# Kernel tuning notes

Hardware: AMD Instinct MI355X
Metric: run time of the kernel (lower is better)

The kernel has to match this reference:

```python
import jax, jax.numpy as jnp
import numpy as np

UNITS = 128
Q_DIM = 256
V_DIM = 256
BATCH = 128
SEQ = 4096


def setup_inputs() -> dict:
    key = jax.random.key(0)
    ks = jax.random.split(key, 8)
    query = jax.random.normal(ks[0], (BATCH, Q_DIM), dtype=jnp.float32)
    values = jax.random.normal(ks[1], (BATCH, SEQ, V_DIM), dtype=jnp.float32)
    # Dense params (glorot-ish scale)
    W1 = jax.random.normal(ks[2], (Q_DIM, UNITS), dtype=jnp.float32) * (1.0 / np.sqrt(Q_DIM))
    b1 = jnp.zeros((UNITS,), dtype=jnp.float32)
    W2 = jax.random.normal(ks[3], (V_DIM, UNITS), dtype=jnp.float32) * (1.0 / np.sqrt(V_DIM))
    b2 = jnp.zeros((UNITS,), dtype=jnp.float32)
    Wv = jax.random.normal(ks[4], (UNITS, 1), dtype=jnp.float32) * (1.0 / np.sqrt(UNITS))
    bv = jnp.zeros((1,), dtype=jnp.float32)
    return {"query": query, "values": values, "W1": W1, "b1": b1,
            "W2": W2, "b2": b2, "Wv": Wv, "bv": bv}


def reference(query, values, W1, b1, W2, b2, Wv, bv):
    # q_proj: [B, 1, U]; v_proj: [B, S, U]
    q_proj = (query @ W1 + b1)[:, None, :]
    v_proj = jnp.einsum('bsd,du->bsu', values, W2) + b2
    # score: [B, S, 1]
    score = jnp.tanh(q_proj + v_proj) @ Wv + bv
    attention_weights = jax.nn.softmax(score, axis=1)  # softmax over seq_len
    context = jnp.sum(attention_weights * values, axis=1)  # [B, V_DIM]
    return (context, attention_weights)
```

## Files before the change

kernel.cpp:

```cpp
#include <hip/hip_runtime.h>

#define B_ 128
#define S_ 4096
#define D_ 256
#define U_ 128
#define SC_ 128
#define CH_ 32

typedef _Float16 half8 __attribute__((ext_vector_type(8)));
typedef _Float16 half4_t __attribute__((ext_vector_type(4)));
typedef float f32x4 __attribute__((ext_vector_type(4)));


__global__ void qp_kernel(const float* __restrict__ query,
                          const float* __restrict__ W1,
                          const float* __restrict__ b1,
                          const float* __restrict__ b2,
                          float* __restrict__ qp) {
  const int idx = blockIdx.x * 256 + threadIdx.x;
  const int b = idx >> 7;
  const int u = idx & 127;
  float acc = b1[u] + b2[u];
  const float* q = query + b * D_;
  #pragma unroll 8
  for (int d = 0; d < D_; ++d) acc += q[d] * W1[d * U_ + u];
  qp[idx] = acc;
}

__global__ void w2t_kernel(const float* __restrict__ W2,
                           _Float16* __restrict__ w2t) {
  const int idx = blockIdx.x * 256 + threadIdx.x;
  const int u = idx >> 8;
  const int d = idx & 255;
  w2t[idx] = (_Float16)W2[d * U_ + u];
}


__global__ __launch_bounds__(256, 1)
void main_kernel(const float* __restrict__ values,
                 const float* __restrict__ qp,
                 const _Float16* __restrict__ w2t,
                 const float* __restrict__ Wv,
                 const float* __restrict__ bv,
                 float* __restrict__ scores,
                 float* __restrict__ part) {
  __shared__ _Float16 Alds[SC_][264];
  __shared__ _Float16 Blds[U_][264];
  __shared__ float sb[2][SC_];
  __shared__ float score_sh[SC_];
  __shared__ float p_sh[SC_];
  __shared__ float qp_sh[U_];
  __shared__ float wv_sh[U_];
  __shared__ float ctxpart[8][D_];
  __shared__ float red[4];

  const int t = threadIdx.x;
  const int bid = blockIdx.x;
  const int b = bid >> 5;
  const int s0 = (bid & 31) * SC_;

  const f32x4* __restrict__ vsrc =
      (const f32x4*)(values + ((size_t)b * S_ + s0) * D_);
  #pragma unroll 8
  for (int i = 0; i < 32; ++i) {
    const int idx = t + i * 256;
    const int row = idx >> 6;
    const int d4 = idx & 63;
    f32x4 v = vsrc[idx];
    half4_t h;
    h[0] = (_Float16)v[0]; h[1] = (_Float16)v[1];
    h[2] = (_Float16)v[2]; h[3] = (_Float16)v[3];
    *(half4_t*)&Alds[row][d4 * 4] = h;
  }
  const half8* __restrict__ wsrc = (const half8*)w2t;
  #pragma unroll 4
  for (int i = 0; i < 16; ++i) {
    const int idx = t + i * 256;
    const int u = idx >> 5;
    const int d8 = idx & 31;
    *(half8*)&Blds[u][d8 * 8] = wsrc[idx];
  }
  if (t < U_) {
    qp_sh[t] = qp[b * U_ + t];
    wv_sh[t] = Wv[t];
  }
  __syncthreads();

  const int lane = t & 63;
  const int wave = t >> 6;
  const int wr = (wave >> 1) * 64;
  const int wcg = wave & 1;
  const int wc = wcg * 64;
  const int lm = lane & 15;
  const int lq = lane >> 4;
  const int lk = lq * 8;

  f32x4 acc[4][4];
  const f32x4 zero = {0.0f, 0.0f, 0.0f, 0.0f};
  #pragma unroll
  for (int mt = 0; mt < 4; ++mt)
    #pragma unroll
    for (int nt = 0; nt < 4; ++nt) acc[mt][nt] = zero;

  #pragma unroll
  for (int k = 0; k < 8; ++k) {
    const int kb = k * 32 + lk;
    half8 af[4], bf[4];
    #pragma unroll
    for (int mt = 0; mt < 4; ++mt)
      af[mt] = *(const half8*)&Alds[wr + mt * 16 + lm][kb];
    #pragma unroll
    for (int nt = 0; nt < 4; ++nt)
      bf[nt] = *(const half8*)&Blds[wc + nt * 16 + lm][kb];
    #pragma unroll
    for (int mt = 0; mt < 4; ++mt)
      #pragma unroll
      for (int nt = 0; nt < 4; ++nt)
        acc[mt][nt] = __builtin_amdgcn_mfma_f32_16x16x32_f16(
            af[mt], bf[nt], acc[mt][nt], 0, 0, 0);
  }

  float qpv[4], wvv[4];
  #pragma unroll
  for (int nt = 0; nt < 4; ++nt) {
    const int u = wc + nt * 16 + lm;
    qpv[nt] = qp_sh[u];
    wvv[nt] = wv_sh[u];
  }
  #pragma unroll
  for (int mt = 0; mt < 4; ++mt) {
    float rs[4] = {0.0f, 0.0f, 0.0f, 0.0f};
    #pragma unroll
    for (int nt = 0; nt < 4; ++nt) {
      #pragma unroll
      for (int r = 0; r < 4; ++r) {
        const float x = acc[mt][nt][r] + qpv[nt];
        const float e = __expf(2.0f * x);
        const float th = 1.0f - 2.0f / (e + 1.0f);
        rs[r] += th * wvv[nt];
      }
    }
    #pragma unroll
    for (int r = 0; r < 4; ++r) {
      float v = rs[r];
      v += __shfl_xor(v, 1);
      v += __shfl_xor(v, 2);
      v += __shfl_xor(v, 4);
      v += __shfl_xor(v, 8);
      if (lm == 0) sb[wcg][wr + mt * 16 + lq * 4 + r] = v;
    }
  }
  __syncthreads();

  if (t < SC_) {
    const float sc = sb[0][t] + sb[1][t] + bv[0];
    scores[(size_t)b * S_ + s0 + t] = sc;
    score_sh[t] = sc;
    float v = sc;
    v = fmaxf(v, __shfl_xor(v, 1));
    v = fmaxf(v, __shfl_xor(v, 2));
    v = fmaxf(v, __shfl_xor(v, 4));
    v = fmaxf(v, __shfl_xor(v, 8));
    v = fmaxf(v, __shfl_xor(v, 16));
    v = fmaxf(v, __shfl_xor(v, 32));
    if ((t & 63) == 0) red[t >> 6] = v;
  }
  __syncthreads();
  const float m_c = fmaxf(red[0], red[1]);
  if (t < SC_) {
    const float pv = __expf(score_sh[t] - m_c);
    p_sh[t] = pv;
    float v = pv;
    v += __shfl_xor(v, 1);
    v += __shfl_xor(v, 2);
    v += __shfl_xor(v, 4);
    v += __shfl_xor(v, 8);
    v += __shfl_xor(v, 16);
    v += __shfl_xor(v, 32);
    if ((t & 63) == 0) red[2 + (t >> 6)] = v;
  }
  __syncthreads();
  const float l_c = red[2] + red[3];

  float cacc[8];
  #pragma unroll
  for (int j = 0; j < 8; ++j) cacc[j] = 0.0f;
  const int v8 = (t & 31) * 8;
  const int rg = t >> 5;
  #pragma unroll
  for (int r = 0; r < 16; ++r) {
    const int row = rg * 16 + r;
    const float pr = p_sh[row];
    half8 hv = *(const half8*)&Alds[row][v8];
    #pragma unroll
    for (int j = 0; j < 8; ++j) cacc[j] += pr * (float)hv[j];
  }
  #pragma unroll
  for (int j = 0; j < 8; ++j) ctxpart[rg][v8 + j] = cacc[j];
  __syncthreads();
  {
    float s = 0.0f;
    #pragma unroll
    for (int g = 0; g < 8; ++g) s += ctxpart[g][t];
    const size_t base = (size_t)bid * 258;
    part[base + 2 + t] = s;
    if (t == 0) { part[base] = m_c; part[base + 1] = l_c; }
  }
}


__global__ void combine_kernel(const float* __restrict__ part,
                               float* __restrict__ ml,
                               float* __restrict__ out_ctx) {
  const int b = blockIdx.x;
  const int t = threadIdx.x;
  float M = -1e30f;
  for (int c = 0; c < CH_; ++c)
    M = fmaxf(M, part[((size_t)(b * CH_ + c)) * 258]);
  float L = 0.0f, s = 0.0f;
  for (int c = 0; c < CH_; ++c) {
    const size_t base = ((size_t)(b * CH_ + c)) * 258;
    const float sc = __expf(part[base] - M);
    L += part[base + 1] * sc;
    s += part[base + 2 + t] * sc;
  }
  out_ctx[b * D_ + t] = s / L;
  if (t == 0) { ml[b * 2] = M; ml[b * 2 + 1] = L; }
}


__global__ void weights_kernel(const float* __restrict__ scores,
                               const float* __restrict__ ml,
                               float* __restrict__ out_w) {
  const int idx = blockIdx.x * 256 + threadIdx.x;
  const int b = idx >> 12;
  const float M = ml[b * 2];
  const float L = ml[b * 2 + 1];
  out_w[idx] = __expf(scores[idx] - M) / L;
}


extern "C" void kernel_launch(void* const* d_in, const int* in_sizes, int n_in,
                              void* d_out, int out_size, void* d_ws, size_t ws_size,
                              hipStream_t stream) {
  const float* query  = (const float*)d_in[0];
  const float* values = (const float*)d_in[1];
  const float* W1     = (const float*)d_in[2];
  const float* b1     = (const float*)d_in[3];
  const float* W2     = (const float*)d_in[4];
  const float* b2     = (const float*)d_in[5];
  const float* Wv     = (const float*)d_in[6];
  const float* bv     = (const float*)d_in[7];

  float* out_ctx = (float*)d_out;
  float* out_w   = out_ctx + B_ * D_;

  char* ws = (char*)d_ws;
  float*     qp     = (float*)ws;
  _Float16*  w2t    = (_Float16*)(ws + 65536);
  float*     scores = (float*)(ws + 131072);
  float*     part   = (float*)(ws + 131072 + 2097152);
  float*     ml     = (float*)(ws + 131072 + 2097152 + 4227072);

  qp_kernel<<<dim3(64), dim3(256), 0, stream>>>(query, W1, b1, b2, qp);
  w2t_kernel<<<dim3(128), dim3(256), 0, stream>>>(W2, w2t);
  main_kernel<<<dim3(B_ * CH_), dim3(256), 0, stream>>>(values, qp, w2t, Wv, bv,
                                                        scores, part);
  combine_kernel<<<dim3(B_), dim3(256), 0, stream>>>(part, ml, out_ctx);
  weights_kernel<<<dim3(B_ * S_ / 256), dim3(256), 0, stream>>>(scores, ml, out_w);
}
```

Before: 836.2 us.

## Stream sequence chunks per block with online softmax and register prefetch

Replaces the 4096 short-lived blocks with 256 persistent 512-thread blocks, each covering half a sequence in 64-row chunks. The next chunk is prefetched into registers while the current one is scored and accumulated, and the softmax and context are updated online. The combine kernel then merges only two partials per batch. This aims to overlap global loads with MFMA and reduction work and to cut launch and partial traffic, at the cost of four barriers per small chunk and limited memory parallelism per CU.

```diff
diff --git a/kernel.cpp b/kernel.cpp
--- a/kernel.cpp
+++ b/kernel.cpp
@@ -4,8 +4,10 @@
 #define S_ 4096
 #define D_ 256
 #define U_ 128
-#define SC_ 128
-#define CH_ 32
+#define CR_ 64
+#define NCH_ 32
+#define HALF_ROWS 2048
+#define PITCH 264
 
 typedef _Float16 half8 __attribute__((ext_vector_type(8)));
 typedef _Float16 half4_t __attribute__((ext_vector_type(4)));
@@ -36,7 +38,7 @@
 }
 
 
-__global__ __launch_bounds__(256, 1)
+__global__ __launch_bounds__(512)
 void main_kernel(const float* __restrict__ values,
                  const float* __restrict__ qp,
                  const _Float16* __restrict__ w2t,
@@ -44,82 +46,59 @@
                  const float* __restrict__ bv,
                  float* __restrict__ scores,
                  float* __restrict__ part) {
-  __shared__ _Float16 Alds[SC_][264];
-  __shared__ _Float16 Blds[U_][264];
-  __shared__ float sb[2][SC_];
-  __shared__ float score_sh[SC_];
-  __shared__ float p_sh[SC_];
+  __shared__ _Float16 Alds[CR_][PITCH];
+  __shared__ _Float16 Blds[U_][PITCH];
+  __shared__ float sb[2][CR_];
+  __shared__ float p_sh[CR_];
   __shared__ float qp_sh[U_];
   __shared__ float wv_sh[U_];
-  __shared__ float ctxpart[8][D_];
-  __shared__ float red[4];
+  __shared__ float ctxpart[16][D_];
+  __shared__ float bc[4];
 
   const int t = threadIdx.x;
-  const int bid = blockIdx.x;
-  const int b = bid >> 5;
-  const int s0 = (bid & 31) * SC_;
-
-  const f32x4* __restrict__ vsrc =
-      (const f32x4*)(values + ((size_t)b * S_ + s0) * D_);
-  #pragma unroll 8
-  for (int i = 0; i < 32; ++i) {
-    const int idx = t + i * 256;
-    const int row = idx >> 6;
-    const int d4 = idx & 63;
-    f32x4 v = vsrc[idx];
-    half4_t h;
-    h[0] = (_Float16)v[0]; h[1] = (_Float16)v[1];
-    h[2] = (_Float16)v[2]; h[3] = (_Float16)v[3];
-    *(half4_t*)&Alds[row][d4 * 4] = h;
-  }
+  const int b = blockIdx.x >> 1;
+  const int half = blockIdx.x & 1;
+  const int lane = t & 63;
+  const int wave = t >> 6;
+
   const half8* __restrict__ wsrc = (const half8*)w2t;
-  #pragma unroll 4
-  for (int i = 0; i < 16; ++i) {
-    const int idx = t + i * 256;
+  #pragma unroll
+  for (int i = 0; i < 8; ++i) {
+    const int idx = t + i * 512;
     const int u = idx >> 5;
     const int d8 = idx & 31;
     *(half8*)&Blds[u][d8 * 8] = wsrc[idx];
   }
-  if (t < U_) {
-    qp_sh[t] = qp[b * U_ + t];
-    wv_sh[t] = Wv[t];
+  if (t < U_) { qp_sh[t] = qp[b * U_ + t]; wv_sh[t] = Wv[t]; }
+  if (t == 0) bc[3] = bv[0];
+
+  const f32x4* __restrict__ vbase =
+      (const f32x4*)(values + ((size_t)b * S_ + half * HALF_ROWS) * D_);
+
+  {
+    f32x4 v[8];
+    #pragma unroll
+    for (int i = 0; i < 8; ++i) v[i] = vbase[t + i * 512];
+    #pragma unroll
+    for (int i = 0; i < 8; ++i) {
+      const int idx = t + i * 512;
+      const int row = idx >> 6;
+      const int d4 = idx & 63;
+      half4_t h;
+      h[0] = (_Float16)v[i][0]; h[1] = (_Float16)v[i][1];
+      h[2] = (_Float16)v[i][2]; h[3] = (_Float16)v[i][3];
+      *(half4_t*)&Alds[row][d4 * 4] = h;
+    }
   }
   __syncthreads();
 
-  const int lane = t & 63;
-  const int wave = t >> 6;
-  const int wr = (wave >> 1) * 64;
+  const int wr = (wave >> 1) * 16;
   const int wcg = wave & 1;
   const int wc = wcg * 64;
   const int lm = lane & 15;
   const int lq = lane >> 4;
   const int lk = lq * 8;
 
-  f32x4 acc[4][4];
-  const f32x4 zero = {0.0f, 0.0f, 0.0f, 0.0f};
-  #pragma unroll
-  for (int mt = 0; mt < 4; ++mt)
-    #pragma unroll
-    for (int nt = 0; nt < 4; ++nt) acc[mt][nt] = zero;
-
-  #pragma unroll
-  for (int k = 0; k < 8; ++k) {
-    const int kb = k * 32 + lk;
-    half8 af[4], bf[4];
-    #pragma unroll
-    for (int mt = 0; mt < 4; ++mt)
-      af[mt] = *(const half8*)&Alds[wr + mt * 16 + lm][kb];
-    #pragma unroll
-    for (int nt = 0; nt < 4; ++nt)
-      bf[nt] = *(const half8*)&Blds[wc + nt * 16 + lm][kb];
-    #pragma unroll
-    for (int mt = 0; mt < 4; ++mt)
-      #pragma unroll
-      for (int nt = 0; nt < 4; ++nt)
-        acc[mt][nt] = __builtin_amdgcn_mfma_f32_16x16x32_f16(
-            af[mt], bf[nt], acc[mt][nt], 0, 0, 0);
-  }
-
   float qpv[4], wvv[4];
   #pragma unroll
   for (int nt = 0; nt < 4; ++nt) {
@@ -127,17 +106,45 @@
     qpv[nt] = qp_sh[u];
     wvv[nt] = wv_sh[u];
   }
-  #pragma unroll
-  for (int mt = 0; mt < 4; ++mt) {
+
+  float M = -INFINITY, L = 0.0f;
+  float cacc[8];
+  #pragma unroll
+  for (int j = 0; j < 8; ++j) cacc[j] = 0.0f;
+  const int rg = t >> 5;
+  const int v8 = (t & 31) * 8;
+
+  for (int c = 0; c < NCH_; ++c) {
+    f32x4 pf[8];
+    if (c + 1 < NCH_) {
+      const f32x4* __restrict__ src = vbase + (size_t)(c + 1) * (CR_ * 64);
+      #pragma unroll
+      for (int i = 0; i < 8; ++i) pf[i] = src[t + i * 512];
+    }
+
+    f32x4 acc[4];
+    const f32x4 zero = {0.0f, 0.0f, 0.0f, 0.0f};
+    #pragma unroll
+    for (int nt = 0; nt < 4; ++nt) acc[nt] = zero;
+    #pragma unroll
+    for (int k = 0; k < 8; ++k) {
+      const int kb = k * 32 + lk;
+      half8 af = *(const half8*)&Alds[wr + lm][kb];
+      #pragma unroll
+      for (int nt = 0; nt < 4; ++nt) {
+        half8 bf = *(const half8*)&Blds[wc + nt * 16 + lm][kb];
+        acc[nt] = __builtin_amdgcn_mfma_f32_16x16x32_f16(af, bf, acc[nt], 0, 0, 0);
+      }
+    }
+
     float rs[4] = {0.0f, 0.0f, 0.0f, 0.0f};
     #pragma unroll
     for (int nt = 0; nt < 4; ++nt) {
       #pragma unroll
       for (int r = 0; r < 4; ++r) {
-        const float x = acc[mt][nt][r] + qpv[nt];
+        const float x = acc[nt][r] + qpv[nt];
         const float e = __expf(2.0f * x);
-        const float th = 1.0f - 2.0f / (e + 1.0f);
-        rs[r] += th * wvv[nt];
+        rs[r] += (1.0f - 2.0f / (e + 1.0f)) * wvv[nt];
       }
     }
     #pragma unroll
@@ -147,64 +154,76 @@
       v += __shfl_xor(v, 2);
       v += __shfl_xor(v, 4);
       v += __shfl_xor(v, 8);
-      if (lm == 0) sb[wcg][wr + mt * 16 + lq * 4 + r] = v;
-    }
-  }
-  __syncthreads();
-
-  if (t < SC_) {
-    const float sc = sb[0][t] + sb[1][t] + bv[0];
-    scores[(size_t)b * S_ + s0 + t] = sc;
-    score_sh[t] = sc;
-    float v = sc;
-    v = fmaxf(v, __shfl_xor(v, 1));
-    v = fmaxf(v, __shfl_xor(v, 2));
-    v = fmaxf(v, __shfl_xor(v, 4));
-    v = fmaxf(v, __shfl_xor(v, 8));
-    v = fmaxf(v, __shfl_xor(v, 16));
-    v = fmaxf(v, __shfl_xor(v, 32));
-    if ((t & 63) == 0) red[t >> 6] = v;
-  }
-  __syncthreads();
-  const float m_c = fmaxf(red[0], red[1]);
-  if (t < SC_) {
-    const float pv = __expf(score_sh[t] - m_c);
-    p_sh[t] = pv;
-    float v = pv;
-    v += __shfl_xor(v, 1);
-    v += __shfl_xor(v, 2);
-    v += __shfl_xor(v, 4);
-    v += __shfl_xor(v, 8);
-    v += __shfl_xor(v, 16);
-    v += __shfl_xor(v, 32);
-    if ((t & 63) == 0) red[2 + (t >> 6)] = v;
-  }
-  __syncthreads();
-  const float l_c = red[2] + red[3];
-
-  float cacc[8];
-  #pragma unroll
-  for (int j = 0; j < 8; ++j) cacc[j] = 0.0f;
-  const int v8 = (t & 31) * 8;
-  const int rg = t >> 5;
-  #pragma unroll
-  for (int r = 0; r < 16; ++r) {
-    const int row = rg * 16 + r;
-    const float pr = p_sh[row];
-    half8 hv = *(const half8*)&Alds[row][v8];
-    #pragma unroll
-    for (int j = 0; j < 8; ++j) cacc[j] += pr * (float)hv[j];
-  }
+      if (lm == 0) sb[wcg][wr + lq * 4 + r] = v;
+    }
+    __syncthreads();
+
+    if (t < CR_) {
+      const float sc = sb[0][t] + sb[1][t] + bc[3];
+      scores[(size_t)b * S_ + half * HALF_ROWS + c * CR_ + t] = sc;
+      float mv = sc;
+      mv = fmaxf(mv, __shfl_xor(mv, 1));
+      mv = fmaxf(mv, __shfl_xor(mv, 2));
+      mv = fmaxf(mv, __shfl_xor(mv, 4));
+      mv = fmaxf(mv, __shfl_xor(mv, 8));
+      mv = fmaxf(mv, __shfl_xor(mv, 16));
+      mv = fmaxf(mv, __shfl_xor(mv, 32));
+      const float m_new = fmaxf(M, mv);
+      const float p = __expf(sc - m_new);
+      p_sh[t] = p;
+      float lv = p;
+      lv += __shfl_xor(lv, 1);
+      lv += __shfl_xor(lv, 2);
+      lv += __shfl_xor(lv, 4);
+      lv += __shfl_xor(lv, 8);
+      lv += __shfl_xor(lv, 16);
+      lv += __shfl_xor(lv, 32);
+      if (t == 0) { bc[0] = m_new; bc[1] = lv; bc[2] = __expf(M - m_new); }
+    }
+    __syncthreads();
+
+    const float alpha = bc[2];
+    const float l_c = bc[1];
+    M = bc[0];
+    L = L * alpha + l_c;
+
+    #pragma unroll
+    for (int j = 0; j < 8; ++j) cacc[j] *= alpha;
+    #pragma unroll
+    for (int r = 0; r < 4; ++r) {
+      const int row = rg * 4 + r;
+      const float pr = p_sh[row];
+      half8 hv = *(const half8*)&Alds[row][v8];
+      #pragma unroll
+      for (int j = 0; j < 8; ++j) cacc[j] += pr * (float)hv[j];
+    }
+    __syncthreads();
+
+    if (c + 1 < NCH_) {
+      #pragma unroll
+      for (int i = 0; i < 8; ++i) {
+        const int idx = t + i * 512;
+        const int row = idx >> 6;
+        const int d4 = idx & 63;
+        half4_t h;
+        h[0] = (_Float16)pf[i][0]; h[1] = (_Float16)pf[i][1];
+        h[2] = (_Float16)pf[i][2]; h[3] = (_Float16)pf[i][3];
+        *(half4_t*)&Alds[row][d4 * 4] = h;
+      }
+    }
+    __syncthreads();
+  }
+
   #pragma unroll
   for (int j = 0; j < 8; ++j) ctxpart[rg][v8 + j] = cacc[j];
   __syncthreads();
-  {
+  if (t < D_) {
     float s = 0.0f;
     #pragma unroll
-    for (int g = 0; g < 8; ++g) s += ctxpart[g][t];
-    const size_t base = (size_t)bid * 258;
+    for (int g = 0; g < 16; ++g) s += ctxpart[g][t];
+    const size_t base = (size_t)blockIdx.x * 258;
     part[base + 2 + t] = s;
-    if (t == 0) { part[base] = m_c; part[base + 1] = l_c; }
+    if (t == 0) { part[base] = M; part[base + 1] = L; }
   }
 }
 
@@ -214,18 +233,16 @@
                                float* __restrict__ out_ctx) {
   const int b = blockIdx.x;
   const int t = threadIdx.x;
-  float M = -1e30f;
-  for (int c = 0; c < CH_; ++c)
-    M = fmaxf(M, part[((size_t)(b * CH_ + c)) * 258]);
-  float L = 0.0f, s = 0.0f;
-  for (int c = 0; c < CH_; ++c) {
-    const size_t base = ((size_t)(b * CH_ + c)) * 258;
-    const float sc = __expf(part[base] - M);
-    L += part[base + 1] * sc;
-    s += part[base + 2 + t] * sc;
-  }
-  out_ctx[b * D_ + t] = s / L;
-  if (t == 0) { ml[b * 2] = M; ml[b * 2 + 1] = L; }
+  const size_t b0 = (size_t)(b * 2) * 258;
+  const size_t b1 = b0 + 258;
+  const float m0 = part[b0], l0 = part[b0 + 1];
+  const float m1 = part[b1], l1 = part[b1 + 1];
+  const float Mf = fmaxf(m0, m1);
+  const float s0 = __expf(m0 - Mf);
+  const float s1 = __expf(m1 - Mf);
+  const float Lf = l0 * s0 + l1 * s1;
+  out_ctx[b * D_ + t] = (part[b0 + 2 + t] * s0 + part[b1 + 2 + t] * s1) / Lf;
+  if (t == 0) { ml[b * 2] = Mf; ml[b * 2 + 1] = Lf; }
 }
 
 
@@ -260,12 +277,12 @@
   _Float16*  w2t    = (_Float16*)(ws + 65536);
   float*     scores = (float*)(ws + 131072);
   float*     part   = (float*)(ws + 131072 + 2097152);
-  float*     ml     = (float*)(ws + 131072 + 2097152 + 4227072);
+  float*     ml     = (float*)(ws + 131072 + 2097152 + 264192);
 
   qp_kernel<<<dim3(64), dim3(256), 0, stream>>>(query, W1, b1, b2, qp);
   w2t_kernel<<<dim3(128), dim3(256), 0, stream>>>(W2, w2t);
-  main_kernel<<<dim3(B_ * CH_), dim3(256), 0, stream>>>(values, qp, w2t, Wv, bv,
-                                                        scores, part);
+  main_kernel<<<dim3(B_ * 2), dim3(512), 0, stream>>>(values, qp, w2t, Wv, bv,
+                                                      scores, part);
   combine_kernel<<<dim3(B_), dim3(256), 0, stream>>>(part, ml, out_ctx);
   weights_kernel<<<dim3(B_ * S_ / 256), dim3(256), 0, stream>>>(scores, ml, out_w);
 }
```

After: 729.6 us. 12.7% less time.
